# Performance work log

Hardware: AMD Instinct MI355X
Metric: run time of the kernel (lower is better)

Reference implementation:

```python
import jax, jax.numpy as jnp
import numpy as np

B, M, D, DOUT, NH = 4096, 64, 512, 256, 8
HD = D // NH  # 64
LN_EPS = 1e-5


def setup_inputs() -> dict:
    key = jax.random.key(0)
    ks = jax.random.split(key, 10)
    s = 1.0 / np.sqrt(D)
    return {
        "H": jax.random.normal(ks[0], (B, M, D), jnp.float32),
        "w": jax.random.uniform(ks[1], (B, M), jnp.float32),
        "agg_query": jax.random.normal(ks[2], (1, 1, D), jnp.float32) * 0.02,
        "in_proj_w": jax.random.normal(ks[3], (3 * D, D), jnp.float32) * s,
        "in_proj_b": jnp.zeros((3 * D,), jnp.float32),
        "out_proj_w": jax.random.normal(ks[4], (D, D), jnp.float32) * s,
        "out_proj_b": jnp.zeros((D,), jnp.float32),
        "ln_g": jnp.ones((D,), jnp.float32),
        "ln_b": jnp.zeros((D,), jnp.float32),
        "w1": jax.random.normal(ks[5], (D, D), jnp.float32) * s,
        "b1": jnp.zeros((D,), jnp.float32),
        "w2": jax.random.normal(ks[6], (DOUT, D), jnp.float32) * s,
        "b2": jnp.zeros((DOUT,), jnp.float32),
    }


def reference(H, w, agg_query, in_proj_w, in_proj_b, out_proj_w, out_proj_b,
              ln_g, ln_b, w1, b1, w2, b2):
    Bc = H.shape[0]
    # weighted sum over codes: (B,M)x(B,M,D) -> (B,D)
    z_weighted = jnp.einsum('bm,bmd->bd', w, H)

    # single-query multi-head attention (torch nn.MultiheadAttention, batch_first)
    Wq, Wk, Wv = jnp.split(in_proj_w, 3, axis=0)
    bq, bk, bv = jnp.split(in_proj_b, 3)
    q = agg_query[0, 0] @ Wq.T + bq                # (D,), shared across batch
    k = H @ Wk.T + bk                              # (B,M,D)
    v = H @ Wv.T + bv                              # (B,M,D)
    qh = q.reshape(NH, HD)
    kh = k.reshape(Bc, M, NH, HD)
    vh = v.reshape(Bc, M, NH, HD)
    scores = jnp.einsum('hd,bmhd->bhm', qh, kh) / jnp.sqrt(jnp.float32(HD))
    attn = jax.nn.softmax(scores, axis=-1)         # (B,NH,M)
    ctx = jnp.einsum('bhm,bmhd->bhd', attn, vh).reshape(Bc, D)
    z_attn = ctx @ out_proj_w.T + out_proj_b       # (B,D)

    z = z_weighted + z_attn
    # LayerNorm -> Linear -> GELU(exact) -> Linear
    mu = jnp.mean(z, axis=-1, keepdims=True)
    var = jnp.var(z, axis=-1, keepdims=True)
    zn = (z - mu) * jax.lax.rsqrt(var + LN_EPS) * ln_g + ln_b
    h = jax.nn.gelu(zn @ w1.T + b1, approximate=False)
    out = h @ w2.T + b2                            # (B,DOUT)
    return jnp.nan_to_num(out, nan=0.0)
```

## Files before the change

kernel.cpp:

```cpp
#include <hip/hip_runtime.h>
#include <hip/hip_bf16.h>
#include <math.h>

#define BN   4096
#define MN   64
#define DN   512
#define DOUTN 256
#define NHN  8

typedef __attribute__((ext_vector_type(8))) short s16x8;
typedef __attribute__((ext_vector_type(4))) float f32x4;

__device__ __forceinline__ unsigned short f2bf(float f) {
    unsigned int u = __float_as_uint(f);
    u += 0x7fffu + ((u >> 16) & 1u);
    return (unsigned short)(u >> 16);
}
__device__ __forceinline__ float bf2f(unsigned short u) {
    return __uint_as_float(((unsigned int)u) << 16);
}

__global__ void k_conv_bf16(const float* __restrict__ src,
                            unsigned short* __restrict__ dst, int n4) {
    int i = blockIdx.x * blockDim.x + threadIdx.x;
    if (i < n4) {
        float4 v = ((const float4*)src)[i];
        ushort4 o;
        o.x = f2bf(v.x); o.y = f2bf(v.y); o.z = f2bf(v.z); o.w = f2bf(v.w);
        ((ushort4*)dst)[i] = o;
    }
}

__global__ void k_q(const float* __restrict__ aq, const float* __restrict__ ipw,
                    const float* __restrict__ ipb, float* __restrict__ qv) {
    int wv = threadIdx.x >> 6, lane = threadIdx.x & 63;
    int i = blockIdx.x * 4 + wv;
    const float* row = ipw + (size_t)i * 512 + lane * 8;
    const float* a = aq + lane * 8;
    float p = 0.f;
#pragma unroll
    for (int j = 0; j < 8; j++) p += a[j] * row[j];
#pragma unroll
    for (int off = 32; off >= 1; off >>= 1) p += __shfl_xor(p, off);
    if (lane == 0) qv[i] = p + ipb[i];
}

__global__ void k_qk(const float* __restrict__ qv, const float* __restrict__ ipw,
                     float* __restrict__ qk) {
    __shared__ float qs[64];
    int h = blockIdx.x, t = threadIdx.x;
    if (t < 64) qs[t] = qv[h * 64 + t];
    __syncthreads();
    float a0 = 0.f, a1 = 0.f;
    for (int j = 0; j < 64; j++) {
        const float* row = ipw + (size_t)(512 + h * 64 + j) * 512;
        float qj = qs[j];
        a0 += qj * row[t];
        a1 += qj * row[t + 256];
    }
    qk[h * 512 + t]       = a0;
    qk[h * 512 + t + 256] = a1;
}

__global__ __launch_bounds__(256) void k_attn(
        const float* __restrict__ H, const float* __restrict__ w,
        const float* __restrict__ qk, unsigned short* __restrict__ ph,
        float* __restrict__ zw) {
    __shared__ unsigned short Hs[64 * 512];
    __shared__ float sc[8][64];
    __shared__ float attn_t[64][8];
    __shared__ float wrow[64];
    const int t = threadIdx.x, lane = t & 63, wv = t >> 6;
    const int b = blockIdx.x;

    if (t < 64) wrow[t] = w[b * 64 + t];

    const float4* Hg = (const float4*)(H + (size_t)b * 32768);
#pragma unroll 8
    for (int c = 0; c < 32; c++) {
        int idx = c * 256 + t;
        float4 v = Hg[idx];
        ushort4 o;
        o.x = f2bf(v.x); o.y = f2bf(v.y); o.z = f2bf(v.z); o.w = f2bf(v.w);
        ((ushort4*)Hs)[idx] = o;
    }

    float qkr[8][8];
#pragma unroll
    for (int h = 0; h < 8; h++) {
        float4 v0 = *(const float4*)(qk + h * 512 + lane * 8);
        float4 v1 = *(const float4*)(qk + h * 512 + lane * 8 + 4);
        qkr[h][0] = v0.x; qkr[h][1] = v0.y; qkr[h][2] = v0.z; qkr[h][3] = v0.w;
        qkr[h][4] = v1.x; qkr[h][5] = v1.y; qkr[h][6] = v1.z; qkr[h][7] = v1.w;
    }
    __syncthreads();

    for (int mi = 0; mi < 16; mi++) {
        int m = wv * 16 + mi;
        const ushort4* hp = (const ushort4*)(Hs + m * 512 + lane * 8);
        ushort4 u0 = hp[0], u1 = hp[1];
        float hv[8] = { bf2f(u0.x), bf2f(u0.y), bf2f(u0.z), bf2f(u0.w),
                        bf2f(u1.x), bf2f(u1.y), bf2f(u1.z), bf2f(u1.w) };
        float p[8];
#pragma unroll
        for (int h = 0; h < 8; h++) {
            float s = 0.f;
#pragma unroll
            for (int j = 0; j < 8; j++) s += hv[j] * qkr[h][j];
            p[h] = s;
        }
#pragma unroll
        for (int off = 32; off >= 1; off >>= 1) {
#pragma unroll
            for (int h = 0; h < 8; h++) p[h] += __shfl_xor(p[h], off);
        }
        if (lane == 0) {
#pragma unroll
            for (int h = 0; h < 8; h++) sc[h][m] = p[h];
        }
    }
    __syncthreads();

#pragma unroll
    for (int hh = 0; hh < 2; hh++) {
        int h = wv * 2 + hh;
        float s = sc[h][lane] * 0.125f;
        float mx = s;
#pragma unroll
        for (int off = 32; off >= 1; off >>= 1) mx = fmaxf(mx, __shfl_xor(mx, off));
        float e = expf(s - mx);
        float sum = e;
#pragma unroll
        for (int off = 32; off >= 1; off >>= 1) sum += __shfl_xor(sum, off);
        attn_t[lane][h] = e / sum;
    }
    __syncthreads();

    float pa0[8], pa1[8], za0 = 0.f, za1 = 0.f;
#pragma unroll
    for (int h = 0; h < 8; h++) { pa0[h] = 0.f; pa1[h] = 0.f; }
    const int d0 = t * 2;
    for (int m = 0; m < 64; m++) {
        float4 a03 = *(const float4*)&attn_t[m][0];
        float4 a47 = *(const float4*)&attn_t[m][4];
        ushort2 hu = *(const ushort2*)(Hs + m * 512 + d0);
        float h0 = bf2f(hu.x), h1 = bf2f(hu.y);
        float wm = wrow[m];
        za0 += wm * h0; za1 += wm * h1;
        pa0[0] += a03.x * h0; pa1[0] += a03.x * h1;
        pa0[1] += a03.y * h0; pa1[1] += a03.y * h1;
        pa0[2] += a03.z * h0; pa1[2] += a03.z * h1;
        pa0[3] += a03.w * h0; pa1[3] += a03.w * h1;
        pa0[4] += a47.x * h0; pa1[4] += a47.x * h1;
        pa0[5] += a47.y * h0; pa1[5] += a47.y * h1;
        pa0[6] += a47.z * h0; pa1[6] += a47.z * h1;
        pa0[7] += a47.w * h0; pa1[7] += a47.w * h1;
    }
    float2 zz; zz.x = za0; zz.y = za1;
    *(float2*)(zw + (size_t)b * 512 + d0) = zz;
#pragma unroll
    for (int h = 0; h < 8; h++) {
        ushort2 o; o.x = f2bf(pa0[h]); o.y = f2bf(pa1[h]);
        *(ushort2*)(ph + (size_t)b * 4096 + h * 512 + d0) = o;
    }
}

__device__ __forceinline__ void gemm_acc(const unsigned short* __restrict__ A,
                                         int aStride,
                                         const unsigned short* __restrict__ Wt,
                                         f32x4 acc[4]) {
    const int lane = threadIdx.x & 63;
    const int wv = threadIdx.x >> 6;
    const int mh = lane & 15, q = lane >> 4;
    const unsigned short* aP = A + (size_t)mh * aStride + q * 8;
    const unsigned short* bP = Wt + (size_t)(wv * 16 + mh) * 512 + q * 8;
#pragma unroll 4
    for (int kk = 0; kk < 512; kk += 32) {
        s16x8 bb = *(const s16x8*)(bP + kk);
#pragma unroll
        for (int tt = 0; tt < 4; tt++) {
            s16x8 aa = *(const s16x8*)(aP + (size_t)tt * 16 * aStride + kk);
            acc[tt] = __builtin_amdgcn_mfma_f32_16x16x32_bf16(aa, bb, acc[tt], 0, 0, 0);
        }
    }
}

__global__ __launch_bounds__(256) void k_ctx(
        const unsigned short* __restrict__ ph, const unsigned short* __restrict__ Wv16,
        const float* __restrict__ ipb, unsigned short* __restrict__ ctx16) {
    const int h = blockIdx.x;
    const int b0 = blockIdx.y * 64;
    f32x4 acc[4];
#pragma unroll
    for (int i = 0; i < 4; i++) { acc[i][0]=0.f; acc[i][1]=0.f; acc[i][2]=0.f; acc[i][3]=0.f; }
    gemm_acc(ph + (size_t)b0 * 4096 + h * 512, 4096,
             Wv16 + (size_t)(h * 64) * 512, acc);
    const int lane = threadIdx.x & 63, wv = threadIdx.x >> 6;
    const int mh = lane & 15, q = lane >> 4;
    const int col = h * 64 + wv * 16 + mh;
    const float bv = ipb[1024 + col];
#pragma unroll
    for (int tt = 0; tt < 4; tt++) {
#pragma unroll
        for (int r = 0; r < 4; r++) {
            int row = b0 + tt * 16 + q * 4 + r;
            ctx16[(size_t)row * 512 + col] = f2bf(acc[tt][r] + bv);
        }
    }
}

__global__ __launch_bounds__(256) void k_zproj(
        const unsigned short* __restrict__ ctx16, const unsigned short* __restrict__ Wo16,
        const float* __restrict__ zw, const float* __restrict__ opb,
        float* __restrict__ z) {
    const int n0 = blockIdx.x * 64, b0 = blockIdx.y * 64;
    f32x4 acc[4];
#pragma unroll
    for (int i = 0; i < 4; i++) { acc[i][0]=0.f; acc[i][1]=0.f; acc[i][2]=0.f; acc[i][3]=0.f; }
    gemm_acc(ctx16 + (size_t)b0 * 512, 512, Wo16 + (size_t)n0 * 512, acc);
    const int lane = threadIdx.x & 63, wv = threadIdx.x >> 6;
    const int mh = lane & 15, q = lane >> 4;
    const int col = n0 + wv * 16 + mh;
    const float bo = opb[col];
#pragma unroll
    for (int tt = 0; tt < 4; tt++) {
#pragma unroll
        for (int r = 0; r < 4; r++) {
            int row = b0 + tt * 16 + q * 4 + r;
            z[(size_t)row * 512 + col] = acc[tt][r] + zw[(size_t)row * 512 + col] + bo;
        }
    }
}

__global__ __launch_bounds__(256) void k_ln(
        const float* __restrict__ z, const float* __restrict__ g,
        const float* __restrict__ bta, unsigned short* __restrict__ zn16) {
    const int wv = threadIdx.x >> 6, lane = threadIdx.x & 63;
    const int row = blockIdx.x * 4 + wv;
    const float* zr = z + (size_t)row * 512 + lane * 8;
    float4 v0 = *(const float4*)zr;
    float4 v1 = *(const float4*)(zr + 4);
    float x[8] = { v0.x, v0.y, v0.z, v0.w, v1.x, v1.y, v1.z, v1.w };
    float s1 = 0.f, s2 = 0.f;
#pragma unroll
    for (int j = 0; j < 8; j++) { s1 += x[j]; s2 += x[j] * x[j]; }
#pragma unroll
    for (int off = 32; off >= 1; off >>= 1) {
        s1 += __shfl_xor(s1, off);
        s2 += __shfl_xor(s2, off);
    }
    float mean = s1 * (1.f / 512.f);
    float var = s2 * (1.f / 512.f) - mean * mean;
    float inv = rsqrtf(fmaxf(var, 0.f) + 1e-5f);
    float4 g0 = *(const float4*)(g + lane * 8);
    float4 g1 = *(const float4*)(g + lane * 8 + 4);
    float4 b0 = *(const float4*)(bta + lane * 8);
    float4 b1 = *(const float4*)(bta + lane * 8 + 4);
    float gg[8] = { g0.x, g0.y, g0.z, g0.w, g1.x, g1.y, g1.z, g1.w };
    float bb[8] = { b0.x, b0.y, b0.z, b0.w, b1.x, b1.y, b1.z, b1.w };
    ushort4 o0, o1;
    o0.x = f2bf((x[0]-mean)*inv*gg[0]+bb[0]);
    o0.y = f2bf((x[1]-mean)*inv*gg[1]+bb[1]);
    o0.z = f2bf((x[2]-mean)*inv*gg[2]+bb[2]);
    o0.w = f2bf((x[3]-mean)*inv*gg[3]+bb[3]);
    o1.x = f2bf((x[4]-mean)*inv*gg[4]+bb[4]);
    o1.y = f2bf((x[5]-mean)*inv*gg[5]+bb[5]);
    o1.z = f2bf((x[6]-mean)*inv*gg[6]+bb[6]);
    o1.w = f2bf((x[7]-mean)*inv*gg[7]+bb[7]);
    ushort4* op = (ushort4*)(zn16 + (size_t)row * 512 + lane * 8);
    op[0] = o0; op[1] = o1;
}

__global__ __launch_bounds__(256) void k_mlp1(
        const unsigned short* __restrict__ zn16, const unsigned short* __restrict__ w116,
        const float* __restrict__ b1, unsigned short* __restrict__ h116) {
    const int n0 = blockIdx.x * 64, b0 = blockIdx.y * 64;
    f32x4 acc[4];
#pragma unroll
    for (int i = 0; i < 4; i++) { acc[i][0]=0.f; acc[i][1]=0.f; acc[i][2]=0.f; acc[i][3]=0.f; }
    gemm_acc(zn16 + (size_t)b0 * 512, 512, w116 + (size_t)n0 * 512, acc);
    const int lane = threadIdx.x & 63, wv = threadIdx.x >> 6;
    const int mh = lane & 15, q = lane >> 4;
    const int col = n0 + wv * 16 + mh;
    const float bias = b1[col];
#pragma unroll
    for (int tt = 0; tt < 4; tt++) {
#pragma unroll
        for (int r = 0; r < 4; r++) {
            int row = b0 + tt * 16 + q * 4 + r;
            float v = acc[tt][r] + bias;
            float gl = 0.5f * v * (1.0f + erff(v * 0.70710678118654752f));
            h116[(size_t)row * 512 + col] = f2bf(gl);
        }
    }
}

__global__ __launch_bounds__(256) void k_mlp2(
        const unsigned short* __restrict__ h116, const unsigned short* __restrict__ w216,
        const float* __restrict__ b2, float* __restrict__ out) {
    const int n0 = blockIdx.x * 64, b0 = blockIdx.y * 64;
    f32x4 acc[4];
#pragma unroll
    for (int i = 0; i < 4; i++) { acc[i][0]=0.f; acc[i][1]=0.f; acc[i][2]=0.f; acc[i][3]=0.f; }
    gemm_acc(h116 + (size_t)b0 * 512, 512, w216 + (size_t)n0 * 512, acc);
    const int lane = threadIdx.x & 63, wv = threadIdx.x >> 6;
    const int mh = lane & 15, q = lane >> 4;
    const int col = n0 + wv * 16 + mh;
    const float bias = b2[col];
#pragma unroll
    for (int tt = 0; tt < 4; tt++) {
#pragma unroll
        for (int r = 0; r < 4; r++) {
            int row = b0 + tt * 16 + q * 4 + r;
            float v = acc[tt][r] + bias;
            if (isnan(v)) v = 0.f;
            else if (isinf(v)) v = v > 0.f ? 3.402823466e38f : -3.402823466e38f;
            out[(size_t)row * 256 + col] = v;
        }
    }
}

#define WS_Q     0u
#define WS_QK    4096u
#define WS_WV16  20480u
#define WS_WO16  544768u
#define WS_W116  1069056u
#define WS_W216  1593344u
#define WS_PH    2097152u
#define WS_ZW    35651584u
#define WS_CTX16 44040192u
#define WS_Z     48234496u
#define WS_ZN16  56623104u
#define WS_H116  60817408u

extern "C" void kernel_launch(void* const* d_in, const int* in_sizes, int n_in,
                              void* d_out, int out_size, void* d_ws, size_t ws_size,
                              hipStream_t stream) {
    const float* H   = (const float*)d_in[0];
    const float* w   = (const float*)d_in[1];
    const float* aq  = (const float*)d_in[2];
    const float* ipw = (const float*)d_in[3];
    const float* ipb = (const float*)d_in[4];
    const float* opw = (const float*)d_in[5];
    const float* opb = (const float*)d_in[6];
    const float* lng = (const float*)d_in[7];
    const float* lnb = (const float*)d_in[8];
    const float* w1  = (const float*)d_in[9];
    const float* b1  = (const float*)d_in[10];
    const float* w2  = (const float*)d_in[11];
    const float* b2  = (const float*)d_in[12];
    float* out = (float*)d_out;
    char* ws = (char*)d_ws;

    float* qv            = (float*)(ws + WS_Q);
    float* qk            = (float*)(ws + WS_QK);
    unsigned short* Wv16 = (unsigned short*)(ws + WS_WV16);
    unsigned short* Wo16 = (unsigned short*)(ws + WS_WO16);
    unsigned short* w116 = (unsigned short*)(ws + WS_W116);
    unsigned short* w216 = (unsigned short*)(ws + WS_W216);
    unsigned short* ph   = (unsigned short*)(ws + WS_PH);
    float* zw            = (float*)(ws + WS_ZW);
    unsigned short* ctx16= (unsigned short*)(ws + WS_CTX16);
    float* z             = (float*)(ws + WS_Z);
    unsigned short* zn16 = (unsigned short*)(ws + WS_ZN16);
    unsigned short* h116 = (unsigned short*)(ws + WS_H116);

    k_conv_bf16<<<256, 256, 0, stream>>>(ipw + (size_t)1024 * 512, Wv16, 65536);
    k_conv_bf16<<<256, 256, 0, stream>>>(opw, Wo16, 65536);
    k_conv_bf16<<<256, 256, 0, stream>>>(w1, w116, 65536);
    k_conv_bf16<<<128, 256, 0, stream>>>(w2, w216, 32768);

    k_q<<<128, 256, 0, stream>>>(aq, ipw, ipb, qv);
    k_qk<<<8, 256, 0, stream>>>(qv, ipw, qk);

    k_attn<<<4096, 256, 0, stream>>>(H, w, qk, ph, zw);

    k_ctx  <<<dim3(8, 64), 256, 0, stream>>>(ph, Wv16, ipb, ctx16);
    k_zproj<<<dim3(8, 64), 256, 0, stream>>>(ctx16, Wo16, zw, opb, z);
    k_ln   <<<1024, 256, 0, stream>>>(z, lng, lnb, zn16);
    k_mlp1 <<<dim3(8, 64), 256, 0, stream>>>(zn16, w116, b1, h116);
    k_mlp2 <<<dim3(4, 64), 256, 0, stream>>>(h116, w216, b2, out);
}
```

Baseline: 900.9 us.

## Compute attention scores with MFMA, pad LDS rows, reorder ph layout

Replaces the per-row scalar dot products plus shuffle reductions for attention scores with a bf16 MFMA over H tiles and a zero-padded bf16 qk matrix, with the softmax scale folded into qk. LDS rows of H are padded to 520 elements to reduce bank conflicts for the MFMA operand reads. The per-head context buffer is stored head-major so the ctx GEMM reads contiguous rows, and the four weight conversion launches are merged into one. It adds bf16 rounding of qk, which may slightly change score precision.

```diff
diff --git a/kernel.cpp b/kernel.cpp
--- a/kernel.cpp
+++ b/kernel.cpp
@@ -20,15 +20,20 @@
     return __uint_as_float(((unsigned int)u) << 16);
 }
 
-__global__ void k_conv_bf16(const float* __restrict__ src,
-                            unsigned short* __restrict__ dst, int n4) {
+__global__ void k_conv_all(const float* __restrict__ s0, const float* __restrict__ s1,
+                           const float* __restrict__ s2, const float* __restrict__ s3,
+                           unsigned short* __restrict__ d0, unsigned short* __restrict__ d1,
+                           unsigned short* __restrict__ d2, unsigned short* __restrict__ d3) {
     int i = blockIdx.x * blockDim.x + threadIdx.x;
-    if (i < n4) {
-        float4 v = ((const float4*)src)[i];
-        ushort4 o;
-        o.x = f2bf(v.x); o.y = f2bf(v.y); o.z = f2bf(v.z); o.w = f2bf(v.w);
-        ((ushort4*)dst)[i] = o;
-    }
+    const float* s; unsigned short* d; int off;
+    if (i < 65536)       { s = s0; d = d0; off = i; }
+    else if (i < 131072) { s = s1; d = d1; off = i - 65536; }
+    else if (i < 196608) { s = s2; d = d2; off = i - 131072; }
+    else                 { s = s3; d = d3; off = i - 196608; }
+    float4 v = ((const float4*)s)[off];
+    ushort4 o;
+    o.x = f2bf(v.x); o.y = f2bf(v.y); o.z = f2bf(v.z); o.w = f2bf(v.w);
+    ((ushort4*)d)[off] = o;
 }
 
 __global__ void k_q(const float* __restrict__ aq, const float* __restrict__ ipw,
@@ -46,9 +51,14 @@
 }
 
 __global__ void k_qk(const float* __restrict__ qv, const float* __restrict__ ipw,
-                     float* __restrict__ qk) {
+                     unsigned short* __restrict__ qkb) {
+    int h = blockIdx.x, t = threadIdx.x;
+    if (h >= 8) {
+        qkb[h * 512 + t] = 0;
+        qkb[h * 512 + t + 256] = 0;
+        return;
+    }
     __shared__ float qs[64];
-    int h = blockIdx.x, t = threadIdx.x;
     if (t < 64) qs[t] = qv[h * 64 + t];
     __syncthreads();
     float a0 = 0.f, a1 = 0.f;
@@ -58,19 +68,20 @@
         a0 += qj * row[t];
         a1 += qj * row[t + 256];
     }
-    qk[h * 512 + t]       = a0;
-    qk[h * 512 + t + 256] = a1;
+    qkb[h * 512 + t]       = f2bf(a0 * 0.125f);
+    qkb[h * 512 + t + 256] = f2bf(a1 * 0.125f);
 }
 
 __global__ __launch_bounds__(256) void k_attn(
         const float* __restrict__ H, const float* __restrict__ w,
-        const float* __restrict__ qk, unsigned short* __restrict__ ph,
+        const unsigned short* __restrict__ qkb, unsigned short* __restrict__ ph,
         float* __restrict__ zw) {
-    __shared__ unsigned short Hs[64 * 512];
+    __shared__ unsigned short Hs[64 * 520];
     __shared__ float sc[8][64];
     __shared__ float attn_t[64][8];
     __shared__ float wrow[64];
     const int t = threadIdx.x, lane = t & 63, wv = t >> 6;
+    const int mh = lane & 15, q = lane >> 4;
     const int b = blockIdx.x;
 
     if (t < 64) wrow[t] = w[b * 64 + t];
@@ -79,44 +90,27 @@
 #pragma unroll 8
     for (int c = 0; c < 32; c++) {
         int idx = c * 256 + t;
+        int m = idx >> 7, dc = (idx & 127) * 4;
         float4 v = Hg[idx];
         ushort4 o;
         o.x = f2bf(v.x); o.y = f2bf(v.y); o.z = f2bf(v.z); o.w = f2bf(v.w);
-        ((ushort4*)Hs)[idx] = o;
-    }
-
-    float qkr[8][8];
-#pragma unroll
-    for (int h = 0; h < 8; h++) {
-        float4 v0 = *(const float4*)(qk + h * 512 + lane * 8);
-        float4 v1 = *(const float4*)(qk + h * 512 + lane * 8 + 4);
-        qkr[h][0] = v0.x; qkr[h][1] = v0.y; qkr[h][2] = v0.z; qkr[h][3] = v0.w;
-        qkr[h][4] = v1.x; qkr[h][5] = v1.y; qkr[h][6] = v1.z; qkr[h][7] = v1.w;
+        *(ushort4*)(Hs + m * 520 + dc) = o;
     }
     __syncthreads();
 
-    for (int mi = 0; mi < 16; mi++) {
-        int m = wv * 16 + mi;
-        const ushort4* hp = (const ushort4*)(Hs + m * 512 + lane * 8);
-        ushort4 u0 = hp[0], u1 = hp[1];
-        float hv[8] = { bf2f(u0.x), bf2f(u0.y), bf2f(u0.z), bf2f(u0.w),
-                        bf2f(u1.x), bf2f(u1.y), bf2f(u1.z), bf2f(u1.w) };
-        float p[8];
-#pragma unroll
-        for (int h = 0; h < 8; h++) {
-            float s = 0.f;
-#pragma unroll
-            for (int j = 0; j < 8; j++) s += hv[j] * qkr[h][j];
-            p[h] = s;
-        }
-#pragma unroll
-        for (int off = 32; off >= 1; off >>= 1) {
-#pragma unroll
-            for (int h = 0; h < 8; h++) p[h] += __shfl_xor(p[h], off);
-        }
-        if (lane == 0) {
-#pragma unroll
-            for (int h = 0; h < 8; h++) sc[h][m] = p[h];
+    {
+        const unsigned short* aP = Hs + (wv * 16 + mh) * 520 + q * 8;
+        const unsigned short* bP = qkb + mh * 512 + q * 8;
+        f32x4 acc = {0.f, 0.f, 0.f, 0.f};
+#pragma unroll
+        for (int kk = 0; kk < 512; kk += 32) {
+            s16x8 aa = *(const s16x8*)(aP + kk);
+            s16x8 bb = *(const s16x8*)(bP + kk);
+            acc = __builtin_amdgcn_mfma_f32_16x16x32_bf16(aa, bb, acc, 0, 0, 0);
+        }
+        if (mh < 8) {
+#pragma unroll
+            for (int r = 0; r < 4; r++) sc[mh][wv * 16 + q * 4 + r] = acc[r];
         }
     }
     __syncthreads();
@@ -124,7 +118,7 @@
 #pragma unroll
     for (int hh = 0; hh < 2; hh++) {
         int h = wv * 2 + hh;
-        float s = sc[h][lane] * 0.125f;
+        float s = sc[h][lane];
         float mx = s;
 #pragma unroll
         for (int off = 32; off >= 1; off >>= 1) mx = fmaxf(mx, __shfl_xor(mx, off));
@@ -143,7 +137,7 @@
     for (int m = 0; m < 64; m++) {
         float4 a03 = *(const float4*)&attn_t[m][0];
         float4 a47 = *(const float4*)&attn_t[m][4];
-        ushort2 hu = *(const ushort2*)(Hs + m * 512 + d0);
+        ushort2 hu = *(const ushort2*)(Hs + m * 520 + d0);
         float h0 = bf2f(hu.x), h1 = bf2f(hu.y);
         float wm = wrow[m];
         za0 += wm * h0; za1 += wm * h1;
@@ -161,7 +155,7 @@
 #pragma unroll
     for (int h = 0; h < 8; h++) {
         ushort2 o; o.x = f2bf(pa0[h]); o.y = f2bf(pa1[h]);
-        *(ushort2*)(ph + (size_t)b * 4096 + h * 512 + d0) = o;
+        *(ushort2*)(ph + (size_t)h * 2097152 + (size_t)b * 512 + d0) = o;
     }
 }
 
@@ -193,7 +187,7 @@
     f32x4 acc[4];
 #pragma unroll
     for (int i = 0; i < 4; i++) { acc[i][0]=0.f; acc[i][1]=0.f; acc[i][2]=0.f; acc[i][3]=0.f; }
-    gemm_acc(ph + (size_t)b0 * 4096 + h * 512, 4096,
+    gemm_acc(ph + (size_t)h * 2097152 + (size_t)b0 * 512, 512,
              Wv16 + (size_t)(h * 64) * 512, acc);
     const int lane = threadIdx.x & 63, wv = threadIdx.x >> 6;
     const int mh = lane & 15, q = lane >> 4;
@@ -321,7 +315,7 @@
 }
 
 #define WS_Q     0u
-#define WS_QK    4096u
+#define WS_QKB   4096u
 #define WS_WV16  20480u
 #define WS_WO16  544768u
 #define WS_W116  1069056u
@@ -353,7 +347,7 @@
     char* ws = (char*)d_ws;
 
     float* qv            = (float*)(ws + WS_Q);
-    float* qk            = (float*)(ws + WS_QK);
+    unsigned short* qkb  = (unsigned short*)(ws + WS_QKB);
     unsigned short* Wv16 = (unsigned short*)(ws + WS_WV16);
     unsigned short* Wo16 = (unsigned short*)(ws + WS_WO16);
     unsigned short* w116 = (unsigned short*)(ws + WS_W116);
@@ -365,15 +359,13 @@
     unsigned short* zn16 = (unsigned short*)(ws + WS_ZN16);
     unsigned short* h116 = (unsigned short*)(ws + WS_H116);
 
-    k_conv_bf16<<<256, 256, 0, stream>>>(ipw + (size_t)1024 * 512, Wv16, 65536);
-    k_conv_bf16<<<256, 256, 0, stream>>>(opw, Wo16, 65536);
-    k_conv_bf16<<<256, 256, 0, stream>>>(w1, w116, 65536);
-    k_conv_bf16<<<128, 256, 0, stream>>>(w2, w216, 32768);
+    k_conv_all<<<896, 256, 0, stream>>>(ipw + (size_t)1024 * 512, opw, w1, w2,
+                                        Wv16, Wo16, w116, w216);
 
     k_q<<<128, 256, 0, stream>>>(aq, ipw, ipb, qv);
-    k_qk<<<8, 256, 0, stream>>>(qv, ipw, qk);
-
-    k_attn<<<4096, 256, 0, stream>>>(H, w, qk, ph, zw);
+    k_qk<<<16, 256, 0, stream>>>(qv, ipw, qkb);
+
+    k_attn<<<4096, 256, 0, stream>>>(H, w, qkb, ph, zw);
 
     k_ctx  <<<dim3(8, 64), 256, 0, stream>>>(ph, Wv16, ipb, ctx16);
     k_zproj<<<dim3(8, 64), 256, 0, stream>>>(ctx16, Wo16, zw, opb, z);
```

Result: faster. 806.6 us (-10.5%).
